# Kernel optimization log

Hardware: AMD Instinct MI355X
Metric: run time of the kernel (lower is better)

## Reference

```python
import jax, jax.numpy as jnp
import numpy as np

B, H, W, CP, CI = 2, 256, 256, 256, 256
IN, OUT = CP + CI, CP          # in_dims=512, out_dims=256
WS, NH, L = 8, 8, 2            # window, heads, num blocks
N = WS * WS                    # tokens per window
HD = OUT // NH                 # head dim = 32
SCALE = HD ** -0.5

def _rel_pos_index():
    c = np.stack(np.meshgrid(np.arange(WS), np.arange(WS), indexing='ij')).reshape(2, -1)
    r = (c[:, :, None] - c[:, None, :]).transpose(1, 2, 0)
    r[..., 0] += WS - 1
    r[..., 1] += WS - 1
    r[..., 0] *= 2 * WS - 1
    return r.sum(-1)  # [N, N] int

REL_IDX = _rel_pos_index()

def _attn_mask(shift):
    img = np.zeros((H, W))
    cnt = 0
    for hs in (slice(0, -WS), slice(-WS, -shift), slice(-shift, None)):
        for ws_ in (slice(0, -WS), slice(-WS, -shift), slice(-shift, None)):
            img[hs, ws_] = cnt
            cnt += 1
    m = img.reshape(H // WS, WS, W // WS, WS).transpose(0, 2, 1, 3).reshape(-1, N)
    d = m[:, None, :] - m[:, :, None]
    return jnp.asarray(np.where(d != 0, -100.0, 0.0).astype(np.float32))  # [nW, N, N]

MASK = _attn_mask(WS // 2)

def _ln(x, g, b, eps=1e-5):
    m = x.mean(-1, keepdims=True)
    v = ((x - m) ** 2).mean(-1, keepdims=True)
    return (x - m) * jax.lax.rsqrt(v + eps) * g + b

def _win_attn(x, qkv_w, qkv_b, rpb_t, proj_w, proj_b, shift):
    # x: [B,H,W,C]
    if shift > 0:
        x = jnp.roll(x, (-shift, -shift), axis=(1, 2))
    nW = (H // WS) * (W // WS)
    xw = x.reshape(B, H // WS, WS, W // WS, WS, OUT).transpose(0, 1, 3, 2, 4, 5).reshape(B, nW, N, OUT)
    qkv = (xw @ qkv_w.T + qkv_b).reshape(B, nW, N, 3, NH, HD)
    q, k, v = qkv[..., 0, :, :], qkv[..., 1, :, :], qkv[..., 2, :, :]  # [B,nW,N,NH,HD]
    attn = jnp.einsum('bwqhd,bwkhd->bwhqk', q * SCALE, k)  # [B,nW,NH,N,N]
    bias = rpb_t[REL_IDX.reshape(-1)].reshape(N, N, NH).transpose(2, 0, 1)  # [NH,N,N]
    attn = attn + bias
    if shift > 0:
        attn = attn + MASK[None, :, None, :, :]
    attn = jax.nn.softmax(attn, axis=-1)
    out = jnp.einsum('bwhqk,bwkhd->bwqhd', attn, v).reshape(B, nW, N, OUT)
    out = out @ proj_w.T + proj_b
    out = out.reshape(B, H // WS, W // WS, WS, WS, OUT).transpose(0, 1, 3, 2, 4, 5).reshape(B, H, W, OUT)
    if shift > 0:
        out = jnp.roll(out, (shift, shift), axis=(1, 2))
    return out

def setup_inputs() -> dict:
    key = jax.random.key(0)
    ks = jax.random.split(key, 12)
    s = 0.02
    p = {}
    p['pcd'] = jax.random.normal(ks[0], (B, H, W, CP), jnp.float32)
    p['img'] = jax.random.normal(ks[1], (B, H, W, CI), jnp.float32)
    p['rd_w1'] = jax.random.normal(ks[2], (4 * IN, IN), jnp.float32) * s
    p['rd_b1'] = jnp.zeros((4 * IN,), jnp.float32)
    p['rd_lng'] = jnp.ones((4 * IN,), jnp.float32)
    p['rd_lnb'] = jnp.zeros((4 * IN,), jnp.float32)
    p['rd_w2'] = jax.random.normal(ks[3], (OUT, 4 * IN), jnp.float32) * s
    p['rd_b2'] = jnp.zeros((OUT,), jnp.float32)
    p['n1g'] = jnp.ones((L, OUT), jnp.float32)
    p['n1b'] = jnp.zeros((L, OUT), jnp.float32)
    p['qkv_w'] = jax.random.normal(ks[4], (L, 3 * OUT, OUT), jnp.float32) * s
    p['qkv_b'] = jnp.zeros((L, 3 * OUT), jnp.float32)
    p['rpb'] = jax.random.normal(ks[5], (L, (2 * WS - 1) ** 2, NH), jnp.float32) * s
    p['proj_w'] = jax.random.normal(ks[6], (L, OUT, OUT), jnp.float32) * s
    p['proj_b'] = jnp.zeros((L, OUT), jnp.float32)
    p['n2g'] = jnp.ones((L, OUT), jnp.float32)
    p['n2b'] = jnp.zeros((L, OUT), jnp.float32)
    p['mlp_w1'] = jax.random.normal(ks[7], (L, 4 * OUT, OUT), jnp.float32) * s
    p['mlp_b1'] = jnp.zeros((L, 4 * OUT), jnp.float32)
    p['mlp_w2'] = jax.random.normal(ks[8], (L, OUT, 4 * OUT), jnp.float32) * s
    p['mlp_b2'] = jnp.zeros((L, OUT), jnp.float32)
    return p

def reference(pcd, img, rd_w1, rd_b1, rd_lng, rd_lnb, rd_w2, rd_b2,
              n1g, n1b, qkv_w, qkv_b, rpb, proj_w, proj_b,
              n2g, n2b, mlp_w1, mlp_b1, mlp_w2, mlp_b2):
    # reduce_dim: Linear -> LeakyReLU(0.01) -> LayerNorm -> Linear
    x = jnp.concatenate([pcd, img], axis=3)
    x = x @ rd_w1.T + rd_b1
    x = jnp.where(x > 0, x, 0.01 * x)
    x = _ln(x, rd_lng, rd_lnb)
    x = x @ rd_w2.T + rd_b2
    # two SwinTransformerBlocks (shift 0, then WS//2)
    for i in range(L):
        shift = 0 if i % 2 == 0 else WS // 2
        x = x + _win_attn(_ln(x, n1g[i], n1b[i]), qkv_w[i], qkv_b[i], rpb[i], proj_w[i], proj_b[i], shift)
        h = _ln(x, n2g[i], n2b[i])
        h = jax.nn.gelu(h @ mlp_w1[i].T + mlp_b1[i], approximate=False)
        x = x + h @ mlp_w2[i].T + mlp_b2[i]
    return x + pcd
```

## Files before the change

### kernel.cpp

```cpp
#include <hip/hip_runtime.h>
#include <math.h>

typedef __attribute__((ext_vector_type(4))) float f32x4v;
typedef __attribute__((ext_vector_type(8))) __bf16 bf16x8v;
typedef __attribute__((ext_vector_type(2))) uint u32x2v;
typedef __attribute__((ext_vector_type(4))) uint u32x4v;

#define SCALE 0.17677669529663687f
#define TOK 131072
#define MCHUNK 32768

__device__ __forceinline__ ushort f2bf(float v){
  uint x = __float_as_uint(v);
  return (ushort)((x + 0x7fffu + ((x >> 16) & 1u)) >> 16);
}
__device__ __forceinline__ float bflo(uint u){ return __uint_as_float(u << 16); }
__device__ __forceinline__ float bfhi(uint u){ return __uint_as_float(u & 0xffff0000u); }
__device__ __forceinline__ float bf2f(ushort u){ return __uint_as_float((uint)u << 16); }

__device__ __forceinline__ void gload16(const void* g, void* l){
  __builtin_amdgcn_global_load_lds(
      (const __attribute__((address_space(1))) uint*)g,
      (__attribute__((address_space(3))) uint*)l, 16, 0, 0);
}

__global__ __launch_bounds__(256) void cvtw_k(const float* __restrict__ src,
    ushort* __restrict__ dst, int n4){
  const int i = blockIdx.x * 256 + threadIdx.x;
  if (i >= n4) return;
  float4 v = ((const float4*)src)[i];
  ushort4 o = { f2bf(v.x), f2bf(v.y), f2bf(v.z), f2bf(v.w) };
  ((ushort4*)dst)[i] = o;
}

__global__ __launch_bounds__(64) void cvtwg_k(const float* __restrict__ src,
    const float* __restrict__ gma, const float* __restrict__ bta,
    ushort* __restrict__ dst, float* __restrict__ c1, float* __restrict__ c2, int K){
  const int n = blockIdx.x, lane = threadIdx.x;
  const float* sp = src + (long)n * K;
  ushort* dp = dst + (long)n * K;
  float s1 = 0.f, s2 = 0.f;
  for (int k = lane * 4; k < K; k += 256){
    float4 wv = *(const float4*)(sp + k);
    float4 gv = *(const float4*)(gma + k);
    float4 bv = *(const float4*)(bta + k);
    s1 += wv.x * gv.x + wv.y * gv.y + wv.z * gv.z + wv.w * gv.w;
    s2 += wv.x * bv.x + wv.y * bv.y + wv.z * bv.z + wv.w * bv.w;
    ushort4 o = { f2bf(wv.x * gv.x), f2bf(wv.y * gv.y), f2bf(wv.z * gv.z), f2bf(wv.w * gv.w) };
    *(ushort4*)(dp + k) = o;
  }
  #pragma unroll
  for (int o = 1; o < 64; o <<= 1){ s1 += __shfl_xor(s1, o); s2 += __shfl_xor(s2, o); }
  if (lane == 0){ c1[n] = s1; c2[n] = s2; }
}

__global__ __launch_bounds__(256) void concat_k(const float* __restrict__ pcd,
    const float* __restrict__ img, ushort* __restrict__ A0){
  const long gid = (long)blockIdx.x * 256 + threadIdx.x;
  const long t = gid >> 7;
  const int c4 = (int)(gid & 127) * 4;
  const float* src = (c4 < 256) ? (pcd + t * 256 + c4) : (img + t * 256 + (c4 - 256));
  float4 v = *(const float4*)src;
  ushort4 o = { f2bf(v.x), f2bf(v.y), f2bf(v.z), f2bf(v.w) };
  __builtin_nontemporal_store(*(u32x2v*)&o, (u32x2v*)(A0 + t * 512 + c4));
}

__global__ __launch_bounds__(256) void rowstats_k(const ushort* __restrict__ X,
    float* __restrict__ stats){
  const int row = blockIdx.x, tid = threadIdx.x;
  uint4 u = *(const uint4*)(X + (long)row * 2048 + tid * 8);
  float s = 0.f, q = 0.f;
  uint* e = (uint*)&u;
  #pragma unroll
  for (int c = 0; c < 4; ++c){
    float a = bflo(e[c]), b2 = bfhi(e[c]);
    s += a + b2; q += a * a + b2 * b2;
  }
  #pragma unroll
  for (int o = 1; o < 64; o <<= 1){ s += __shfl_xor(s, o); q += __shfl_xor(q, o); }
  __shared__ float ss[4], qs[4];
  if ((tid & 63) == 0){ ss[tid >> 6] = s; qs[tid >> 6] = q; }
  __syncthreads();
  if (tid == 0){
    float S = ss[0] + ss[1] + ss[2] + ss[3];
    float Q = qs[0] + qs[1] + qs[2] + qs[3];
    float mean = S * (1.f / 2048.f);
    float var = Q * (1.f / 2048.f) - mean * mean;
    stats[row * 2] = mean;
    stats[row * 2 + 1] = rsqrtf(var + 1e-5f);
  }
}

__global__ __launch_bounds__(256) void stats256b_k(const ushort* __restrict__ xb,
    float* __restrict__ stats){
  const int lane = threadIdx.x & 63, wd = threadIdx.x >> 6;
  const long row = (long)blockIdx.x * 4 + wd;
  uint2 u = *(const uint2*)(xb + row * 256 + lane * 4);
  float a = bflo(u.x), b2 = bfhi(u.x), c = bflo(u.y), d = bfhi(u.y);
  float s = a + b2 + c + d;
  float q = a * a + b2 * b2 + c * c + d * d;
  #pragma unroll
  for (int o = 1; o < 64; o <<= 1){ s += __shfl_xor(s, o); q += __shfl_xor(q, o); }
  if (lane == 0){
    float mean = s * (1.f / 256.f);
    float var = q * (1.f / 256.f) - mean * mean;
    stats[row * 2] = mean;
    stats[row * 2 + 1] = rsqrtf(var + 1e-5f);
  }
}

template<int ACT, int OUTT, int RES, bool LNEPI, int MINB>
__global__ __launch_bounds__(256, MINB) void gemm_k(
    const ushort* __restrict__ A, const ushort* __restrict__ W,
    const float* __restrict__ bias,
    float* __restrict__ outf, ushort* __restrict__ outb,
    const ushort* __restrict__ res, const float* __restrict__ pcdp,
    const float* __restrict__ stats, const float* __restrict__ c1v,
    const float* __restrict__ c2v, int N, int K, int gx)
{
  __shared__ ushort As[2][128 * 32];
  __shared__ ushort Bs[2][128 * 32];
  const int tid = threadIdx.x;
  const int lane = tid & 63, w = tid >> 6;
  const int nwg = gridDim.x;
  {
    const int xcd = blockIdx.x & 7;
    const int idx = blockIdx.x >> 3;
    const int mPerX = nwg / (8 * gx);
    const int sg = idx / (8 * gx);
    const int u  = idx - sg * (8 * gx);
    const int nT = u >> 3;
    const int ml = u & 7;
    const int mT = xcd * mPerX + sg * 8 + ml;
    const int mBase = mT * 128;
    const int nBase = nT * 128;
    const int fr = lane & 15, grp = lane >> 4;
    const int wr = w >> 1, wc = w & 1;

    f32x4v acc[4][4];
    #pragma unroll
    for (int i = 0; i < 4; ++i)
      #pragma unroll
      for (int j = 0; j < 4; ++j) acc[i][j] = (f32x4v){0.f, 0.f, 0.f, 0.f};

    const ushort* Ap = A + (long)(mBase + w * 32 + (lane >> 2)) * K + (lane & 3) * 8;
    const ushort* Wp = W + (long)(nBase + w * 32 + (lane >> 2)) * K + (lane & 3) * 8;
    const long rowstep = (long)16 * K;
    const int woff = (w * 32) * 32;

    gload16(Ap, &As[0][woff]);
    gload16(Ap + rowstep, &As[0][woff + 512]);
    gload16(Wp, &Bs[0][woff]);
    gload16(Wp + rowstep, &Bs[0][woff + 512]);
    Ap += 32; Wp += 32;
    __syncthreads();

    int cur = 0;
    for (int kt = 0; kt < K; kt += 32){
      if (kt + 32 < K){
        const int nxt = cur ^ 1;
        gload16(Ap, &As[nxt][woff]);
        gload16(Ap + rowstep, &As[nxt][woff + 512]);
        gload16(Wp, &Bs[nxt][woff]);
        gload16(Wp + rowstep, &Bs[nxt][woff + 512]);
        Ap += 32; Wp += 32;
      }
      bf16x8v af[4], bv[4];
      #pragma unroll
      for (int i = 0; i < 4; ++i)
        af[i] = *(const bf16x8v*)&As[cur][(wr * 64 + i * 16 + fr) * 32 + grp * 8];
      #pragma unroll
      for (int j = 0; j < 4; ++j)
        bv[j] = *(const bf16x8v*)&Bs[cur][(wc * 64 + j * 16 + fr) * 32 + grp * 8];
      #pragma unroll
      for (int i = 0; i < 4; ++i)
        #pragma unroll
        for (int j = 0; j < 4; ++j)
          acc[i][j] = __builtin_amdgcn_mfma_f32_16x16x32_bf16(af[i], bv[j], acc[i][j], 0, 0, 0);
      __syncthreads();
      cur ^= 1;
    }

    float muv[16], rsv[16];
    if (LNEPI){
      #pragma unroll
      for (int i = 0; i < 4; ++i)
        #pragma unroll
        for (int rr = 0; rr < 4; ++rr){
          const int m = mBase + wr * 64 + i * 16 + grp * 4 + rr;
          muv[i * 4 + rr] = stats[m * 2];
          rsv[i * 4 + rr] = stats[m * 2 + 1];
        }
    }
    #pragma unroll
    for (int j = 0; j < 4; ++j){
      const int n = nBase + wc * 64 + j * 16 + fr;
      const float bn = bias[n];
      float c1n = 0.f, c2n = 0.f;
      if (LNEPI){ c1n = c1v[n]; c2n = c2v[n]; }
      #pragma unroll
      for (int i = 0; i < 4; ++i){
        #pragma unroll
        for (int rr = 0; rr < 4; ++rr){
          const long m = mBase + wr * 64 + i * 16 + grp * 4 + rr;
          float v = acc[i][j][rr];
          if (LNEPI) v = rsv[i * 4 + rr] * v - muv[i * 4 + rr] * rsv[i * 4 + rr] * c1n + c2n;
          v += bn;
          if (ACT == 1) v = v > 0.f ? v : 0.01f * v;
          if (ACT == 2){
            const float u2 = v * (0.7978845608f + 0.0356774081f * v * v);
            const float t = 1.f - 2.f / (__expf(2.f * u2) + 1.f);
            v = 0.5f * v * (1.f + t);
          }
          if (RES >= 1) v += bf2f(res[m * N + n]);
          if (RES == 2) v += pcdp[m * N + n];
          acc[i][j][rr] = v;
          if (OUTT == 0) __builtin_nontemporal_store(v, &outf[m * N + n]);
        }
      }
    }
    if (OUTT == 1){
      ushort* eb = &As[0][0];
      __syncthreads();
      #pragma unroll
      for (int p = 0; p < 2; ++p){
        if (wr == p){
          #pragma unroll
          for (int i = 0; i < 4; ++i)
            #pragma unroll
            for (int rr = 0; rr < 4; ++rr){
              const int rl = i * 16 + grp * 4 + rr;
              #pragma unroll
              for (int j = 0; j < 4; ++j)
                eb[rl * 128 + wc * 64 + j * 16 + fr] = f2bf(acc[i][j][rr]);
            }
        }
        __syncthreads();
        #pragma unroll
        for (int it = 0; it < 4; ++it){
          const int c = it * 256 + tid;
          const int row = c >> 4, col = (c & 15) * 8;
          const u32x4v val = *(const u32x4v*)&eb[row * 128 + col];
          __builtin_nontemporal_store(val,
              (u32x4v*)(outb + (long)(mBase + p * 64 + row) * N + nBase + col));
        }
        __syncthreads();
      }
    }
  }
}

template<int SHIFT>
__global__ __launch_bounds__(256) void attn_k(const ushort* __restrict__ qkv,
    const float* __restrict__ rpb, ushort* __restrict__ outp)
{
  __shared__ float Kf[64][132];
  __shared__ float Vf[64][132];
  __shared__ float bias_s[4][226];
  __shared__ int code_s[64];
  const int tid = threadIdx.x;
  const int lane = tid & 63, wid = tid >> 6;
  const int hg = blockIdx.x & 1;
  const int bw = blockIdx.x >> 1;
  const int b = bw >> 10, widx = bw & 1023;
  const int wh = widx >> 5, ww = widx & 31;
  const int head = hg * 4 + wid;

  for (int i = lane; i < 225; i += 64) bias_s[wid][i] = rpb[i * 8 + head];

  if (SHIFT > 0 && tid < 64){
    const int hh = wh * 8 + (tid >> 3), wwp = ww * 8 + (tid & 7);
    const int rh = (hh < 248) ? 0 : ((hh < 256 - SHIFT) ? 1 : 2);
    const int rw = (wwp < 248) ? 0 : ((wwp < 256 - SHIFT) ? 1 : 2);
    code_s[tid] = rh * 3 + rw;
  }

  #pragma unroll
  for (int it = 0; it < 4; ++it){
    const int c = it * 256 + tid;
    const int row = c >> 4, part = c & 15;
    const int hs = (wh * 8 + (row >> 3) + SHIFT) & 255;
    const int wsm = (ww * 8 + (row & 7) + SHIFT) & 255;
    const long tk = ((long)b * 256 + hs) * 256 + wsm;
    const uint4 ku = *(const uint4*)(qkv + tk * 768 + 256 + hg * 128 + part * 8);
    const uint4 vu = *(const uint4*)(qkv + tk * 768 + 512 + hg * 128 + part * 8);
    const uint* ke = (const uint*)&ku;
    const uint* ve = (const uint*)&vu;
    #pragma unroll
    for (int e = 0; e < 4; ++e){
      Kf[row][part * 8 + e * 2]     = bflo(ke[e]);
      Kf[row][part * 8 + e * 2 + 1] = bfhi(ke[e]);
      Vf[row][part * 8 + e * 2]     = bflo(ve[e]);
      Vf[row][part * 8 + e * 2 + 1] = bfhi(ve[e]);
    }
  }

  const int th = lane >> 3, tw = lane & 7;
  const int h = wh * 8 + th, w = ww * 8 + tw;
  int mycode = 0;
  if (SHIFT > 0){
    const int rh = (h < 248) ? 0 : ((h < 256 - SHIFT) ? 1 : 2);
    const int rw = (w < 248) ? 0 : ((w < 256 - SHIFT) ? 1 : 2);
    mycode = rh * 3 + rw;
  }
  const int hs = (h + SHIFT) & 255;
  const int wsm = (w + SHIFT) & 255;
  const long tok = ((long)b * 256 + hs) * 256 + wsm;
  const ushort* qb = qkv + tok * 768 + head * 32;
  float q[32];
  #pragma unroll
  for (int d2 = 0; d2 < 16; ++d2){
    const uint u = *(const uint*)(qb + d2 * 2);
    q[d2 * 2]     = bflo(u) * SCALE;
    q[d2 * 2 + 1] = bfhi(u) * SCALE;
  }
  __syncthreads();

  const int hb = wid * 32;
  f32x4v o[8];
  #pragma unroll
  for (int d4 = 0; d4 < 8; ++d4) o[d4] = (f32x4v){0.f, 0.f, 0.f, 0.f};
  float sum = 0.f;
  for (int k = 0; k < 64; ++k){
    float s0 = 0.f, s1 = 0.f, s2 = 0.f, s3 = 0.f;
    #pragma unroll
    for (int d4 = 0; d4 < 8; ++d4){
      const f32x4v kv = *(const f32x4v*)&Kf[k][hb + d4 * 4];
      s0 += q[d4 * 4 + 0] * kv[0];
      s1 += q[d4 * 4 + 1] * kv[1];
      s2 += q[d4 * 4 + 2] * kv[2];
      s3 += q[d4 * 4 + 3] * kv[3];
    }
    float s = (s0 + s1) + (s2 + s3);
    s += bias_s[wid][(th - (k >> 3) + 7) * 15 + (tw - (k & 7) + 7)];
    if (SHIFT > 0 && mycode != code_s[k]) s -= 100.f;
    const float p = __expf(s);
    sum += p;
    #pragma unroll
    for (int d4 = 0; d4 < 8; ++d4){
      const f32x4v vv = *(const f32x4v*)&Vf[k][hb + d4 * 4];
      o[d4] += p * vv;
    }
  }
  const float inv = 1.f / sum;
  ushort* ob = outp + tok * 256 + head * 32;
  #pragma unroll
  for (int d4 = 0; d4 < 8; ++d4){
    ushort4 ov = { f2bf(o[d4][0] * inv), f2bf(o[d4][1] * inv),
                   f2bf(o[d4][2] * inv), f2bf(o[d4][3] * inv) };
    *(ushort4*)(ob + d4 * 4) = ov;
  }
}

extern "C" void kernel_launch(void* const* d_in, const int* in_sizes, int n_in,
                              void* d_out, int out_size, void* d_ws, size_t ws_size,
                              hipStream_t stream){
  const float* pcd    = (const float*)d_in[0];
  const float* img    = (const float*)d_in[1];
  const float* rd_w1  = (const float*)d_in[2];
  const float* rd_b1  = (const float*)d_in[3];
  const float* rd_lng = (const float*)d_in[4];
  const float* rd_lnb = (const float*)d_in[5];
  const float* rd_w2  = (const float*)d_in[6];
  const float* rd_b2  = (const float*)d_in[7];
  const float* n1g    = (const float*)d_in[8];
  const float* n1b    = (const float*)d_in[9];
  const float* qkv_w  = (const float*)d_in[10];
  const float* qkv_b  = (const float*)d_in[11];
  const float* rpb    = (const float*)d_in[12];
  const float* proj_w = (const float*)d_in[13];
  const float* proj_b = (const float*)d_in[14];
  const float* n2g    = (const float*)d_in[15];
  const float* n2b    = (const float*)d_in[16];
  const float* mlp_w1 = (const float*)d_in[17];
  const float* mlp_b1 = (const float*)d_in[18];
  const float* mlp_w2 = (const float*)d_in[19];
  const float* mlp_b2 = (const float*)d_in[20];

  char* ws = (char*)d_ws;
  ushort* w1b    = (ushort*)(ws + 0);
  ushort* w2g    = (ushort*)(ws + 2097152);
  ushort* qkvwg  = (ushort*)(ws + 3145728);
  ushort* projwb = (ushort*)(ws + 3932160);
  ushort* mlp1wg = (ushort*)(ws + 4194304);
  ushort* mlp2wb = (ushort*)(ws + 5242880);
  float*  cvec   = (float*)(ws + 6291456);
  float*  w2c1   = cvec,        *w2c2   = cvec + 256;
  float*  qkvc1  = cvec + 512,  *qkvc2  = cvec + 2048;
  float*  mlp1c1 = cvec + 3584, *mlp1c2 = cvec + 5632;
  float*  stats  = (float*)(ws + 6324224);
  ushort* xr     = (ushort*)(ws + 7372800);
  char*   big    = ws + 74481664;
  ushort* A0     = (ushort*)big;
  ushort* X1c    = (ushort*)(big + 134217728);
  ushort* qkvb   = (ushort*)big;
  ushort* attno  = (ushort*)(big + 201326592);
  ushort* hidden = (ushort*)big;
  float* xout = (float*)d_out;

  cvtw_k<<<1024, 256, 0, stream>>>(rd_w1, w1b, 262144);
  cvtw_k<<<128,  256, 0, stream>>>(proj_w, projwb, 32768);
  cvtw_k<<<512,  256, 0, stream>>>(mlp_w2, mlp2wb, 131072);
  cvtwg_k<<<256, 64, 0, stream>>>(rd_w2, rd_lng, rd_lnb, w2g, w2c1, w2c2, 2048);
  for (int i = 0; i < 2; ++i){
    cvtwg_k<<<768, 64, 0, stream>>>(qkv_w + i * 196608, n1g + i * 256, n1b + i * 256,
        qkvwg + i * 196608, qkvc1 + i * 768, qkvc2 + i * 768, 256);
    cvtwg_k<<<1024, 64, 0, stream>>>(mlp_w1 + i * 262144, n2g + i * 256, n2b + i * 256,
        mlp1wg + i * 262144, mlp1c1 + i * 1024, mlp1c2 + i * 1024, 256);
  }
  concat_k<<<65536, 256, 0, stream>>>(pcd, img, A0);

  for (int c = 0; c < 4; ++c){
    const long off = (long)c * MCHUNK;
    gemm_k<1,1,0,false,2><<<4096, 256, 0, stream>>>(A0 + off * 512, w1b, rd_b1,
        nullptr, X1c, nullptr, nullptr, nullptr, nullptr, nullptr, 2048, 512, 16);
    rowstats_k<<<MCHUNK, 256, 0, stream>>>(X1c, stats + off * 2);
    gemm_k<0,1,0,true,2><<<512, 256, 0, stream>>>(X1c, w2g, rd_b2,
        nullptr, xr + off * 256, nullptr, nullptr,
        stats + off * 2, w2c1, w2c2, 256, 2048, 2);
  }
  stats256b_k<<<TOK / 4, 256, 0, stream>>>(xr, stats);

  for (int i = 0; i < 2; ++i){
    gemm_k<0,1,0,true,2><<<6144, 256, 0, stream>>>(xr, qkvwg + i * 196608, qkv_b + i * 768,
        nullptr, qkvb, nullptr, nullptr, stats, qkvc1 + i * 768, qkvc2 + i * 768,
        768, 256, 6);
    if (i == 0)
      attn_k<0><<<4096, 256, 0, stream>>>(qkvb, rpb, attno);
    else
      attn_k<4><<<4096, 256, 0, stream>>>(qkvb, rpb + 1800, attno);
    gemm_k<0,1,1,false,2><<<2048, 256, 0, stream>>>(attno, projwb + i * 65536,
        proj_b + i * 256, nullptr, xr, xr, nullptr, nullptr, nullptr, nullptr, 256, 256, 2);
    stats256b_k<<<TOK / 4, 256, 0, stream>>>(xr, stats);
    gemm_k<2,1,0,true,2><<<8192, 256, 0, stream>>>(xr, mlp1wg + i * 262144,
        mlp_b1 + i * 1024, nullptr, hidden, nullptr, nullptr,
        stats, mlp1c1 + i * 1024, mlp1c2 + i * 1024, 1024, 256, 8);
    if (i == 0){
      gemm_k<0,1,1,false,2><<<2048, 256, 0, stream>>>(hidden, mlp2wb, mlp_b2,
          nullptr, xr, xr, nullptr, nullptr, nullptr, nullptr, 256, 1024, 2);
      stats256b_k<<<TOK / 4, 256, 0, stream>>>(xr, stats);
    } else {
      gemm_k<0,0,2,false,2><<<2048, 256, 0, stream>>>(hidden, mlp2wb + 262144,
          mlp_b2 + 256, xout, nullptr, xr, pcd, nullptr, nullptr, nullptr, 256, 1024, 2);
    }
  }
}
```

Baseline: 2.102 ms.

## Store activations and weights in K-blocked 32-column panel layout

Moves all bf16 activations and weights to a panel-major layout, where each 32-wide K slice of all rows is stored contiguously. This lets each GEMM tile load read a contiguous 2KB block instead of strided 64-byte row pieces. The conversion, stats, attention and epilogue indexing are all rewritten to match. The risk is that attention and stats reads now touch several distant panels per token, which may hurt their coalescing.

```diff
diff --git a/kernel.cpp b/kernel.cpp
--- a/kernel.cpp
+++ b/kernel.cpp
@@ -9,6 +9,8 @@
 #define SCALE 0.17677669529663687f
 #define TOK 131072
 #define MCHUNK 32768
+#define T32 ((long)TOK * 32)
+#define C32 ((long)MCHUNK * 32)
 
 __device__ __forceinline__ ushort f2bf(float v){
   uint x = __float_as_uint(v);
@@ -25,20 +27,22 @@
 }
 
 __global__ __launch_bounds__(256) void cvtw_k(const float* __restrict__ src,
-    ushort* __restrict__ dst, int n4){
+    ushort* __restrict__ dst, int K, long m32, int n4){
   const int i = blockIdx.x * 256 + threadIdx.x;
   if (i >= n4) return;
+  const int flat = i * 4;
+  const int r = flat / K, k = flat % K;
   float4 v = ((const float4*)src)[i];
   ushort4 o = { f2bf(v.x), f2bf(v.y), f2bf(v.z), f2bf(v.w) };
-  ((ushort4*)dst)[i] = o;
+  *(ushort4*)(dst + (long)(k >> 5) * m32 + (long)r * 32 + (k & 31)) = o;
 }
 
 __global__ __launch_bounds__(64) void cvtwg_k(const float* __restrict__ src,
     const float* __restrict__ gma, const float* __restrict__ bta,
-    ushort* __restrict__ dst, float* __restrict__ c1, float* __restrict__ c2, int K){
+    ushort* __restrict__ dst, float* __restrict__ c1, float* __restrict__ c2,
+    int K, long m32){
   const int n = blockIdx.x, lane = threadIdx.x;
   const float* sp = src + (long)n * K;
-  ushort* dp = dst + (long)n * K;
   float s1 = 0.f, s2 = 0.f;
   for (int k = lane * 4; k < K; k += 256){
     float4 wv = *(const float4*)(sp + k);
@@ -47,7 +51,7 @@
     s1 += wv.x * gv.x + wv.y * gv.y + wv.z * gv.z + wv.w * gv.w;
     s2 += wv.x * bv.x + wv.y * bv.y + wv.z * bv.z + wv.w * bv.w;
     ushort4 o = { f2bf(wv.x * gv.x), f2bf(wv.y * gv.y), f2bf(wv.z * gv.z), f2bf(wv.w * gv.w) };
-    *(ushort4*)(dp + k) = o;
+    *(ushort4*)(dst + (long)(k >> 5) * m32 + (long)n * 32 + (k & 31)) = o;
   }
   #pragma unroll
   for (int o = 1; o < 64; o <<= 1){ s1 += __shfl_xor(s1, o); s2 += __shfl_xor(s2, o); }
@@ -62,13 +66,15 @@
   const float* src = (c4 < 256) ? (pcd + t * 256 + c4) : (img + t * 256 + (c4 - 256));
   float4 v = *(const float4*)src;
   ushort4 o = { f2bf(v.x), f2bf(v.y), f2bf(v.z), f2bf(v.w) };
-  __builtin_nontemporal_store(*(u32x2v*)&o, (u32x2v*)(A0 + t * 512 + c4));
+  const long chunk = t >> 15, tc = t & 32767;
+  ushort* dst = A0 + chunk * 16777216 + (long)(c4 >> 5) * C32 + tc * 32 + (c4 & 31);
+  __builtin_nontemporal_store(*(u32x2v*)&o, (u32x2v*)dst);
 }
 
 __global__ __launch_bounds__(256) void rowstats_k(const ushort* __restrict__ X,
     float* __restrict__ stats){
   const int row = blockIdx.x, tid = threadIdx.x;
-  uint4 u = *(const uint4*)(X + (long)row * 2048 + tid * 8);
+  uint4 u = *(const uint4*)(X + (long)(tid >> 2) * C32 + (long)row * 32 + (tid & 3) * 8);
   float s = 0.f, q = 0.f;
   uint* e = (uint*)&u;
   #pragma unroll
@@ -95,7 +101,7 @@
     float* __restrict__ stats){
   const int lane = threadIdx.x & 63, wd = threadIdx.x >> 6;
   const long row = (long)blockIdx.x * 4 + wd;
-  uint2 u = *(const uint2*)(xb + row * 256 + lane * 4);
+  uint2 u = *(const uint2*)(xb + (long)(lane >> 3) * T32 + row * 32 + (lane & 7) * 4);
   float a = bflo(u.x), b2 = bfhi(u.x), c = bflo(u.y), d = bfhi(u.y);
   float s = a + b2 + c + d;
   float q = a * a + b2 * b2 + c * c + d * d;
@@ -116,136 +122,136 @@
     float* __restrict__ outf, ushort* __restrict__ outb,
     const ushort* __restrict__ res, const float* __restrict__ pcdp,
     const float* __restrict__ stats, const float* __restrict__ c1v,
-    const float* __restrict__ c2v, int N, int K, int gx)
+    const float* __restrict__ c2v, int N, int K, int gx,
+    long aM32, long wM32, long oM32, int mOff)
 {
   __shared__ ushort As[2][128 * 32];
   __shared__ ushort Bs[2][128 * 32];
   const int tid = threadIdx.x;
   const int lane = tid & 63, w = tid >> 6;
   const int nwg = gridDim.x;
-  {
-    const int xcd = blockIdx.x & 7;
-    const int idx = blockIdx.x >> 3;
-    const int mPerX = nwg / (8 * gx);
-    const int sg = idx / (8 * gx);
-    const int u  = idx - sg * (8 * gx);
-    const int nT = u >> 3;
-    const int ml = u & 7;
-    const int mT = xcd * mPerX + sg * 8 + ml;
-    const int mBase = mT * 128;
-    const int nBase = nT * 128;
-    const int fr = lane & 15, grp = lane >> 4;
-    const int wr = w >> 1, wc = w & 1;
-
-    f32x4v acc[4][4];
+  const int xcd = blockIdx.x & 7;
+  const int idx = blockIdx.x >> 3;
+  const int mPerX = nwg / (8 * gx);
+  const int sg = idx / (8 * gx);
+  const int u  = idx - sg * (8 * gx);
+  const int nT = u >> 3;
+  const int ml = u & 7;
+  const int mBase = (xcd * mPerX + sg * 8 + ml) * 128;
+  const int nBase = nT * 128;
+  const int fr = lane & 15, grp = lane >> 4;
+  const int wr = w >> 1, wc = w & 1;
+
+  f32x4v acc[4][4];
+  #pragma unroll
+  for (int i = 0; i < 4; ++i)
+    #pragma unroll
+    for (int j = 0; j < 4; ++j) acc[i][j] = (f32x4v){0.f, 0.f, 0.f, 0.f};
+
+  const long aBase = (long)(mBase + w * 32) * 32 + lane * 8;
+  const long wBase = (long)(nBase + w * 32) * 32 + lane * 8;
+  const int woff = w * 1024;
+
+  gload16(A + aBase, &As[0][woff]);
+  gload16(A + aBase + 512, &As[0][woff + 512]);
+  gload16(W + wBase, &Bs[0][woff]);
+  gload16(W + wBase + 512, &Bs[0][woff + 512]);
+  __syncthreads();
+
+  const int NT = K >> 5;
+  int cur = 0;
+  for (int t = 0; t < NT; ++t){
+    if (t + 1 < NT){
+      const long ao = aBase + (long)(t + 1) * aM32;
+      const long wo = wBase + (long)(t + 1) * wM32;
+      const int nxt = cur ^ 1;
+      gload16(A + ao, &As[nxt][woff]);
+      gload16(A + ao + 512, &As[nxt][woff + 512]);
+      gload16(W + wo, &Bs[nxt][woff]);
+      gload16(W + wo + 512, &Bs[nxt][woff + 512]);
+    }
+    bf16x8v af[4], bv[4];
+    #pragma unroll
+    for (int i = 0; i < 4; ++i)
+      af[i] = *(const bf16x8v*)&As[cur][(wr * 64 + i * 16 + fr) * 32 + grp * 8];
+    #pragma unroll
+    for (int j = 0; j < 4; ++j)
+      bv[j] = *(const bf16x8v*)&Bs[cur][(wc * 64 + j * 16 + fr) * 32 + grp * 8];
     #pragma unroll
     for (int i = 0; i < 4; ++i)
       #pragma unroll
-      for (int j = 0; j < 4; ++j) acc[i][j] = (f32x4v){0.f, 0.f, 0.f, 0.f};
-
-    const ushort* Ap = A + (long)(mBase + w * 32 + (lane >> 2)) * K + (lane & 3) * 8;
-    const ushort* Wp = W + (long)(nBase + w * 32 + (lane >> 2)) * K + (lane & 3) * 8;
-    const long rowstep = (long)16 * K;
-    const int woff = (w * 32) * 32;
-
-    gload16(Ap, &As[0][woff]);
-    gload16(Ap + rowstep, &As[0][woff + 512]);
-    gload16(Wp, &Bs[0][woff]);
-    gload16(Wp + rowstep, &Bs[0][woff + 512]);
-    Ap += 32; Wp += 32;
+      for (int j = 0; j < 4; ++j)
+        acc[i][j] = __builtin_amdgcn_mfma_f32_16x16x32_bf16(af[i], bv[j], acc[i][j], 0, 0, 0);
     __syncthreads();
-
-    int cur = 0;
-    for (int kt = 0; kt < K; kt += 32){
-      if (kt + 32 < K){
-        const int nxt = cur ^ 1;
-        gload16(Ap, &As[nxt][woff]);
-        gload16(Ap + rowstep, &As[nxt][woff + 512]);
-        gload16(Wp, &Bs[nxt][woff]);
-        gload16(Wp + rowstep, &Bs[nxt][woff + 512]);
-        Ap += 32; Wp += 32;
+    cur ^= 1;
+  }
+
+  float muv[16], rsv[16];
+  if (LNEPI){
+    #pragma unroll
+    for (int i = 0; i < 4; ++i)
+      #pragma unroll
+      for (int rr = 0; rr < 4; ++rr){
+        const int m = mBase + wr * 64 + i * 16 + grp * 4 + rr;
+        muv[i * 4 + rr] = stats[m * 2];
+        rsv[i * 4 + rr] = stats[m * 2 + 1];
       }
-      bf16x8v af[4], bv[4];
+  }
+  #pragma unroll
+  for (int j = 0; j < 4; ++j){
+    const int n = nBase + wc * 64 + j * 16 + fr;
+    const float bn = bias[n];
+    float c1n = 0.f, c2n = 0.f;
+    if (LNEPI){ c1n = c1v[n]; c2n = c2v[n]; }
+    #pragma unroll
+    for (int i = 0; i < 4; ++i){
       #pragma unroll
-      for (int i = 0; i < 4; ++i)
-        af[i] = *(const bf16x8v*)&As[cur][(wr * 64 + i * 16 + fr) * 32 + grp * 8];
-      #pragma unroll
-      for (int j = 0; j < 4; ++j)
-        bv[j] = *(const bf16x8v*)&Bs[cur][(wc * 64 + j * 16 + fr) * 32 + grp * 8];
-      #pragma unroll
-      for (int i = 0; i < 4; ++i)
+      for (int rr = 0; rr < 4; ++rr){
+        const long m = mBase + wr * 64 + i * 16 + grp * 4 + rr;
+        float v = acc[i][j][rr];
+        if (LNEPI) v = rsv[i * 4 + rr] * v - muv[i * 4 + rr] * rsv[i * 4 + rr] * c1n + c2n;
+        v += bn;
+        if (ACT == 1) v = v > 0.f ? v : 0.01f * v;
+        if (ACT == 2){
+          const float u2 = v * (0.7978845608f + 0.0356774081f * v * v);
+          const float t2 = 1.f - 2.f / (__expf(2.f * u2) + 1.f);
+          v = 0.5f * v * (1.f + t2);
+        }
+        if (RES >= 1)
+          v += bf2f(res[(long)(n >> 5) * T32 + (mOff + m) * 32 + (n & 31)]);
+        if (RES == 2) v += pcdp[(mOff + m) * N + n];
+        acc[i][j][rr] = v;
+        if (OUTT == 0) __builtin_nontemporal_store(v, &outf[(mOff + m) * N + n]);
+      }
+    }
+  }
+  if (OUTT == 1){
+    ushort* eb = &As[0][0];
+    __syncthreads();
+    #pragma unroll
+    for (int p = 0; p < 2; ++p){
+      if (wr == p){
         #pragma unroll
-        for (int j = 0; j < 4; ++j)
-          acc[i][j] = __builtin_amdgcn_mfma_f32_16x16x32_bf16(af[i], bv[j], acc[i][j], 0, 0, 0);
-      __syncthreads();
-      cur ^= 1;
-    }
-
-    float muv[16], rsv[16];
-    if (LNEPI){
-      #pragma unroll
-      for (int i = 0; i < 4; ++i)
-        #pragma unroll
-        for (int rr = 0; rr < 4; ++rr){
-          const int m = mBase + wr * 64 + i * 16 + grp * 4 + rr;
-          muv[i * 4 + rr] = stats[m * 2];
-          rsv[i * 4 + rr] = stats[m * 2 + 1];
-        }
-    }
-    #pragma unroll
-    for (int j = 0; j < 4; ++j){
-      const int n = nBase + wc * 64 + j * 16 + fr;
-      const float bn = bias[n];
-      float c1n = 0.f, c2n = 0.f;
-      if (LNEPI){ c1n = c1v[n]; c2n = c2v[n]; }
-      #pragma unroll
-      for (int i = 0; i < 4; ++i){
-        #pragma unroll
-        for (int rr = 0; rr < 4; ++rr){
-          const long m = mBase + wr * 64 + i * 16 + grp * 4 + rr;
-          float v = acc[i][j][rr];
-          if (LNEPI) v = rsv[i * 4 + rr] * v - muv[i * 4 + rr] * rsv[i * 4 + rr] * c1n + c2n;
-          v += bn;
-          if (ACT == 1) v = v > 0.f ? v : 0.01f * v;
-          if (ACT == 2){
-            const float u2 = v * (0.7978845608f + 0.0356774081f * v * v);
-            const float t = 1.f - 2.f / (__expf(2.f * u2) + 1.f);
-            v = 0.5f * v * (1.f + t);
+        for (int i = 0; i < 4; ++i)
+          #pragma unroll
+          for (int rr = 0; rr < 4; ++rr){
+            const int rl = i * 16 + grp * 4 + rr;
+            #pragma unroll
+            for (int j = 0; j < 4; ++j)
+              eb[rl * 128 + wc * 64 + j * 16 + fr] = f2bf(acc[i][j][rr]);
           }
-          if (RES >= 1) v += bf2f(res[m * N + n]);
-          if (RES == 2) v += pcdp[m * N + n];
-          acc[i][j][rr] = v;
-          if (OUTT == 0) __builtin_nontemporal_store(v, &outf[m * N + n]);
-        }
       }
-    }
-    if (OUTT == 1){
-      ushort* eb = &As[0][0];
       __syncthreads();
       #pragma unroll
-      for (int p = 0; p < 2; ++p){
-        if (wr == p){
-          #pragma unroll
-          for (int i = 0; i < 4; ++i)
-            #pragma unroll
-            for (int rr = 0; rr < 4; ++rr){
-              const int rl = i * 16 + grp * 4 + rr;
-              #pragma unroll
-              for (int j = 0; j < 4; ++j)
-                eb[rl * 128 + wc * 64 + j * 16 + fr] = f2bf(acc[i][j][rr]);
-            }
-        }
-        __syncthreads();
-        #pragma unroll
-        for (int it = 0; it < 4; ++it){
-          const int c = it * 256 + tid;
-          const int row = c >> 4, col = (c & 15) * 8;
-          const u32x4v val = *(const u32x4v*)&eb[row * 128 + col];
-          __builtin_nontemporal_store(val,
-              (u32x4v*)(outb + (long)(mBase + p * 64 + row) * N + nBase + col));
-        }
-        __syncthreads();
+      for (int it = 0; it < 4; ++it){
+        const int c = it * 256 + tid;
+        const int row = c >> 4, cg = c & 15;
+        const u32x4v val = *(const u32x4v*)&eb[row * 128 + cg * 8];
+        ushort* dst = outb + (long)((nBase >> 5) + (cg >> 2)) * oM32
+                    + (long)(mOff + mBase + p * 64 + row) * 32 + (cg & 3) * 8;
+        __builtin_nontemporal_store(val, (u32x4v*)dst);
       }
+      __syncthreads();
     }
   }
 }
@@ -282,16 +288,18 @@
     const int hs = (wh * 8 + (row >> 3) + SHIFT) & 255;
     const int wsm = (ww * 8 + (row & 7) + SHIFT) & 255;
     const long tk = ((long)b * 256 + hs) * 256 + wsm;
-    const uint4 ku = *(const uint4*)(qkv + tk * 768 + 256 + hg * 128 + part * 8);
-    const uint4 vu = *(const uint4*)(qkv + tk * 768 + 512 + hg * 128 + part * 8);
+    const long sub = tk * 32 + (part & 3) * 8;
+    const uint4 ku = *(const uint4*)(qkv + (long)(8  + hg * 4 + (part >> 2)) * T32 + sub);
+    const uint4 vu = *(const uint4*)(qkv + (long)(16 + hg * 4 + (part >> 2)) * T32 + sub);
     const uint* ke = (const uint*)&ku;
     const uint* ve = (const uint*)&vu;
+    const int col = (part >> 2) * 32 + (part & 3) * 8;
     #pragma unroll
     for (int e = 0; e < 4; ++e){
-      Kf[row][part * 8 + e * 2]     = bflo(ke[e]);
-      Kf[row][part * 8 + e * 2 + 1] = bfhi(ke[e]);
-      Vf[row][part * 8 + e * 2]     = bflo(ve[e]);
-      Vf[row][part * 8 + e * 2 + 1] = bfhi(ve[e]);
+      Kf[row][col + e * 2]     = bflo(ke[e]);
+      Kf[row][col + e * 2 + 1] = bfhi(ke[e]);
+      Vf[row][col + e * 2]     = bflo(ve[e]);
+      Vf[row][col + e * 2 + 1] = bfhi(ve[e]);
     }
   }
 
@@ -306,7 +314,7 @@
   const int hs = (h + SHIFT) & 255;
   const int wsm = (w + SHIFT) & 255;
   const long tok = ((long)b * 256 + hs) * 256 + wsm;
-  const ushort* qb = qkv + tok * 768 + head * 32;
+  const ushort* qb = qkv + (long)head * T32 + tok * 32;
   float q[32];
   #pragma unroll
   for (int d2 = 0; d2 < 16; ++d2){
@@ -343,7 +351,7 @@
     }
   }
   const float inv = 1.f / sum;
-  ushort* ob = outp + tok * 256 + head * 32;
+  ushort* ob = outp + (long)head * T32 + tok * 32;
   #pragma unroll
   for (int d4 = 0; d4 < 8; ++d4){
     ushort4 ov = { f2bf(o[d4][0] * inv), f2bf(o[d4][1] * inv),
@@ -398,50 +406,56 @@
   ushort* hidden = (ushort*)big;
   float* xout = (float*)d_out;
 
-  cvtw_k<<<1024, 256, 0, stream>>>(rd_w1, w1b, 262144);
-  cvtw_k<<<128,  256, 0, stream>>>(proj_w, projwb, 32768);
-  cvtw_k<<<512,  256, 0, stream>>>(mlp_w2, mlp2wb, 131072);
-  cvtwg_k<<<256, 64, 0, stream>>>(rd_w2, rd_lng, rd_lnb, w2g, w2c1, w2c2, 2048);
+  cvtw_k<<<1024, 256, 0, stream>>>(rd_w1, w1b, 512, 65536, 262144);
+  cvtwg_k<<<256, 64, 0, stream>>>(rd_w2, rd_lng, rd_lnb, w2g, w2c1, w2c2, 2048, 8192);
   for (int i = 0; i < 2; ++i){
+    cvtw_k<<<64,  256, 0, stream>>>(proj_w + i * 65536, projwb + i * 65536, 256, 8192, 16384);
+    cvtw_k<<<256, 256, 0, stream>>>(mlp_w2 + i * 262144, mlp2wb + i * 262144, 1024, 8192, 65536);
     cvtwg_k<<<768, 64, 0, stream>>>(qkv_w + i * 196608, n1g + i * 256, n1b + i * 256,
-        qkvwg + i * 196608, qkvc1 + i * 768, qkvc2 + i * 768, 256);
+        qkvwg + i * 196608, qkvc1 + i * 768, qkvc2 + i * 768, 256, 24576);
     cvtwg_k<<<1024, 64, 0, stream>>>(mlp_w1 + i * 262144, n2g + i * 256, n2b + i * 256,
-        mlp1wg + i * 262144, mlp1c1 + i * 1024, mlp1c2 + i * 1024, 256);
+        mlp1wg + i * 262144, mlp1c1 + i * 1024, mlp1c2 + i * 1024, 256, 32768);
   }
   concat_k<<<65536, 256, 0, stream>>>(pcd, img, A0);
 
   for (int c = 0; c < 4; ++c){
     const long off = (long)c * MCHUNK;
-    gemm_k<1,1,0,false,2><<<4096, 256, 0, stream>>>(A0 + off * 512, w1b, rd_b1,
-        nullptr, X1c, nullptr, nullptr, nullptr, nullptr, nullptr, 2048, 512, 16);
+    gemm_k<1,1,0,false,2><<<4096, 256, 0, stream>>>(A0 + (long)c * 16777216, w1b, rd_b1,
+        nullptr, X1c, nullptr, nullptr, nullptr, nullptr, nullptr,
+        2048, 512, 16, C32, 65536, C32, 0);
     rowstats_k<<<MCHUNK, 256, 0, stream>>>(X1c, stats + off * 2);
     gemm_k<0,1,0,true,2><<<512, 256, 0, stream>>>(X1c, w2g, rd_b2,
-        nullptr, xr + off * 256, nullptr, nullptr,
-        stats + off * 2, w2c1, w2c2, 256, 2048, 2);
+        nullptr, xr, nullptr, nullptr,
+        stats + off * 2, w2c1, w2c2,
+        256, 2048, 2, C32, 8192, T32, (int)off);
   }
   stats256b_k<<<TOK / 4, 256, 0, stream>>>(xr, stats);
 
   for (int i = 0; i < 2; ++i){
     gemm_k<0,1,0,true,2><<<6144, 256, 0, stream>>>(xr, qkvwg + i * 196608, qkv_b + i * 768,
         nullptr, qkvb, nullptr, nullptr, stats, qkvc1 + i * 768, qkvc2 + i * 768,
-        768, 256, 6);
+        768, 256, 6, T32, 24576, T32, 0);
     if (i == 0)
       attn_k<0><<<4096, 256, 0, stream>>>(qkvb, rpb, attno);
     else
       attn_k<4><<<4096, 256, 0, stream>>>(qkvb, rpb + 1800, attno);
     gemm_k<0,1,1,false,2><<<2048, 256, 0, stream>>>(attno, projwb + i * 65536,
-        proj_b + i * 256, nullptr, xr, xr, nullptr, nullptr, nullptr, nullptr, 256, 256, 2);
+        proj_b + i * 256, nullptr, xr, xr, nullptr, nullptr, nullptr, nullptr,
+        256, 256, 2, T32, 8192, T32, 0);
     stats256b_k<<<TOK / 4, 256, 0, stream>>>(xr, stats);
     gemm_k<2,1,0,true,2><<<8192, 256, 0, stream>>>(xr, mlp1wg + i * 262144,
         mlp_b1 + i * 1024, nullptr, hidden, nullptr, nullptr,
-        stats, mlp1c1 + i * 1024, mlp1c2 + i * 1024, 1024, 256, 8);
+        stats, mlp1c1 + i * 1024, mlp1c2 + i * 1024,
+        1024, 256, 8, T32, 32768, T32, 0);
     if (i == 0){
       gemm_k<0,1,1,false,2><<<2048, 256, 0, stream>>>(hidden, mlp2wb, mlp_b2,
-          nullptr, xr, xr, nullptr, nullptr, nullptr, nullptr, 256, 1024, 2);
+          nullptr, xr, xr, nullptr, nullptr, nullptr, nullptr,
+          256, 1024, 2, T32, 8192, T32, 0);
       stats256b_k<<<TOK / 4, 256, 0, stream>>>(xr, stats);
     } else {
       gemm_k<0,0,2,false,2><<<2048, 256, 0, stream>>>(hidden, mlp2wb + 262144,
-          mlp_b2 + 256, xout, nullptr, xr, pcd, nullptr, nullptr, nullptr, 256, 1024, 2);
-    }
-  }
-}
+          mlp_b2 + 256, xout, nullptr, xr, pcd, nullptr, nullptr, nullptr,
+          256, 1024, 2, T32, 8192, T32, 0);
+    }
+  }
+}
```

After: 2.176 ms. 1.04x slower.
